# Optimization experiments

Measured on AMD Instinct MI355X. Metric: run time of the kernel, lower is better.

The kernel has to match this reference:

```python
import jax, jax.numpy as jnp
import numpy as np

T, B, V, H = 256, 256, 512, 1024


def setup_inputs() -> dict:
    key = jax.random.key(0)
    k1, k2, k3, k4 = jax.random.split(key, 4)
    # lecun_normal-like scaling for stability
    return {
        "inputs": jax.random.normal(k1, (T, B, V), dtype=jnp.float32),
        "W_xh": jax.random.normal(k2, (V, H), dtype=jnp.float32) / np.sqrt(V),
        "W_hh": jax.random.normal(k3, (H, H), dtype=jnp.float32) / np.sqrt(H),
        "b_h": jnp.zeros((H,), dtype=jnp.float32),
        "W_dense": jax.random.normal(k4, (H, V), dtype=jnp.float32) / np.sqrt(H),
        "b_dense": jnp.zeros((V,), dtype=jnp.float32),
    }


def reference(inputs, W_xh, W_hh, b_h, W_dense, b_dense):
    # Pre-compute the input projection for all timesteps (one big GEMM).
    xh = jnp.einsum("tbv,vh->tbh", inputs, W_xh) + b_h  # [T, B, H]

    def step(h, x_t):
        h_new = jnp.tanh(x_t + jnp.matmul(h, W_hh))
        return h_new, h_new

    h0 = jnp.zeros((inputs.shape[1], W_hh.shape[0]), dtype=inputs.dtype)
    state, hs = jax.lax.scan(step, h0, xh)  # hs: [T, B, H]

    outputs = jnp.einsum("tbh,hv->tbv", hs, W_dense) + b_dense  # [T, B, V]
    return outputs, state
```

## Files before the change

### kernel.cpp

```cpp
#include <hip/hip_runtime.h>


#define T_STEPS 256
#define B_SZ    256
#define V_SZ    512
#define H_SZ    1024
#define BH      (B_SZ * H_SZ)
#define M1      (T_STEPS * B_SZ)

typedef __attribute__((ext_vector_type(8))) short bf16x8;
typedef __attribute__((ext_vector_type(4))) float f32x4;

__device__ inline unsigned short bf16_rne(float f) {
    unsigned u = __float_as_uint(f);
    u += 0x7fffu + ((u >> 16) & 1u);
    return (unsigned short)(u >> 16);
}

__global__ __launch_bounds__(256, 4)
void gemm_f32_xh(const float* __restrict__ A, const float* __restrict__ Bw,
                 const float* __restrict__ bias, float* __restrict__ C)
{
    __shared__ __align__(16) float As[16][128];
    __shared__ __align__(16) float Bs[16][128];
    const int tid = threadIdx.x;
    const int tx = tid & 15, ty = tid >> 4;
    const int r0 = blockIdx.y * 128, c0 = blockIdx.x * 128;
    const int ar = tid >> 1, ak = (tid & 1) * 8;
    const int bk = tid >> 4, bc = (tid & 15) * 8;

    float acc[8][8] = {};

    for (int kc = 0; kc < V_SZ; kc += 16) {
        const float* ap = A + (size_t)(r0 + ar) * V_SZ + kc + ak;
        float4 a0 = ((const float4*)ap)[0];
        float4 a1 = ((const float4*)ap)[1];
        const float* bp = Bw + (size_t)(kc + bk) * H_SZ + c0 + bc;
        float4 b0 = ((const float4*)bp)[0];
        float4 b1 = ((const float4*)bp)[1];
        __syncthreads();
        As[ak + 0][ar] = a0.x; As[ak + 1][ar] = a0.y;
        As[ak + 2][ar] = a0.z; As[ak + 3][ar] = a0.w;
        As[ak + 4][ar] = a1.x; As[ak + 5][ar] = a1.y;
        As[ak + 6][ar] = a1.z; As[ak + 7][ar] = a1.w;
        *(float4*)&Bs[bk][bc]     = b0;
        *(float4*)&Bs[bk][bc + 4] = b1;
        __syncthreads();
#pragma unroll
        for (int kk = 0; kk < 16; ++kk) {
            float ra[8], rb[8];
            *(float4*)(ra)     = *(const float4*)&As[kk][ty * 8];
            *(float4*)(ra + 4) = *(const float4*)&As[kk][ty * 8 + 4];
            *(float4*)(rb)     = *(const float4*)&Bs[kk][tx * 8];
            *(float4*)(rb + 4) = *(const float4*)&Bs[kk][tx * 8 + 4];
#pragma unroll
            for (int i = 0; i < 8; ++i)
#pragma unroll
                for (int j = 0; j < 8; ++j)
                    acc[i][j] += ra[i] * rb[j];
        }
    }

    float4 bv0 = *(const float4*)(bias + c0 + tx * 8);
    float4 bv1 = *(const float4*)(bias + c0 + tx * 8 + 4);
#pragma unroll
    for (int i = 0; i < 8; ++i) {
        float* cp = C + (size_t)(r0 + ty * 8 + i) * H_SZ + c0 + tx * 8;
        float4 o0, o1;
        o0.x = acc[i][0] + bv0.x; o0.y = acc[i][1] + bv0.y;
        o0.z = acc[i][2] + bv0.z; o0.w = acc[i][3] + bv0.w;
        o1.x = acc[i][4] + bv1.x; o1.y = acc[i][5] + bv1.y;
        o1.z = acc[i][6] + bv1.z; o1.w = acc[i][7] + bv1.w;
        ((float4*)cp)[0] = o0;
        ((float4*)cp)[1] = o1;
    }
}

__global__ __launch_bounds__(512, 2)
void scan_gemm(const float* __restrict__ Hprev, const float* __restrict__ Whh,
               float* __restrict__ P)
{
    __shared__ __align__(16) float As[16][68];
    __shared__ __align__(16) float Bs[16][128];
    const int tid = threadIdx.x;
    const int tx = tid & 31, ty = tid >> 5;
    const int c0 = blockIdx.x * 128;
    const int r0 = blockIdx.y * 64;
    const int k0 = blockIdx.z * 128;
    const int ar = tid >> 3, ak = (tid & 7) * 2;
    const int bk = tid >> 5, bc = (tid & 31) * 4;

    float acc[4][4] = {};

    for (int kc = 0; kc < 128; kc += 16) {
        float2 a2 = *(const float2*)(Hprev + (size_t)(r0 + ar) * H_SZ + k0 + kc + ak);
        float4 b4 = *(const float4*)(Whh + (size_t)(k0 + kc + bk) * H_SZ + c0 + bc);
        __syncthreads();
        As[ak][ar]     = a2.x;
        As[ak + 1][ar] = a2.y;
        *(float4*)&Bs[bk][bc] = b4;
        __syncthreads();
#pragma unroll
        for (int kk = 0; kk < 16; ++kk) {
            float4 ra = *(const float4*)&As[kk][ty * 4];
            float4 rb = *(const float4*)&Bs[kk][tx * 4];
            acc[0][0] += ra.x * rb.x; acc[0][1] += ra.x * rb.y;
            acc[0][2] += ra.x * rb.z; acc[0][3] += ra.x * rb.w;
            acc[1][0] += ra.y * rb.x; acc[1][1] += ra.y * rb.y;
            acc[1][2] += ra.y * rb.z; acc[1][3] += ra.y * rb.w;
            acc[2][0] += ra.z * rb.x; acc[2][1] += ra.z * rb.y;
            acc[2][2] += ra.z * rb.z; acc[2][3] += ra.z * rb.w;
            acc[3][0] += ra.w * rb.x; acc[3][1] += ra.w * rb.y;
            acc[3][2] += ra.w * rb.z; acc[3][3] += ra.w * rb.w;
        }
    }

    float* pp = P + (size_t)blockIdx.z * BH;
#pragma unroll
    for (int i = 0; i < 4; ++i) {
        float4 o; o.x = acc[i][0]; o.y = acc[i][1]; o.z = acc[i][2]; o.w = acc[i][3];
        *(float4*)(pp + (size_t)(r0 + ty * 4 + i) * H_SZ + c0 + tx * 4) = o;
    }
}

__global__ __launch_bounds__(256)
void scan_reduce(const float* __restrict__ P, float* __restrict__ XH)
{
    int i = (blockIdx.x * 256 + threadIdx.x) * 4;
    float4 s = *(const float4*)(XH + i);
#pragma unroll
    for (int ks = 0; ks < 8; ++ks) {
        float4 p = *(const float4*)(P + (size_t)ks * BH + i);
        s.x += p.x; s.y += p.y; s.z += p.z; s.w += p.w;
    }
    float4 o;
    o.x = tanhf(s.x); o.y = tanhf(s.y); o.z = tanhf(s.z); o.w = tanhf(s.w);
    *(float4*)(XH + i) = o;
}

__global__ __launch_bounds__(256)
void tanh_inplace(float* __restrict__ X)
{
    int i = (blockIdx.x * 256 + threadIdx.x) * 4;
    float4 x = *(float4*)(X + i);
    float4 o;
    o.x = tanhf(x.x); o.y = tanhf(x.y); o.z = tanhf(x.z); o.w = tanhf(x.w);
    *(float4*)(X + i) = o;
}

__global__ __launch_bounds__(256)
void cvt_wdense(const float* __restrict__ Wd, unsigned short* __restrict__ WdT)
{
    __shared__ float tile[64][65];
    const int tid = threadIdx.x;
    const int kt = blockIdx.x * 64, nt = blockIdx.y * 64;
    const int kr = tid >> 2, nc = (tid & 3) * 16;
#pragma unroll
    for (int i = 0; i < 4; ++i) {
        float4 v = *(const float4*)(Wd + (size_t)(kt + kr) * V_SZ + nt + nc + i * 4);
        tile[kr][nc + i * 4 + 0] = v.x;
        tile[kr][nc + i * 4 + 1] = v.y;
        tile[kr][nc + i * 4 + 2] = v.z;
        tile[kr][nc + i * 4 + 3] = v.w;
    }
    __syncthreads();
    const int nr = tid >> 2, kc = (tid & 3) * 16;
    unsigned words[8];
#pragma unroll
    for (int j = 0; j < 8; ++j) {
        unsigned short lo = bf16_rne(tile[kc + 2 * j][nr]);
        unsigned short hi = bf16_rne(tile[kc + 2 * j + 1][nr]);
        words[j] = (unsigned)lo | ((unsigned)hi << 16);
    }
    unsigned* wp = (unsigned*)(WdT + (size_t)(nt + nr) * H_SZ + kt + kc);
    ((uint4*)wp)[0] = make_uint4(words[0], words[1], words[2], words[3]);
    ((uint4*)wp)[1] = make_uint4(words[4], words[5], words[6], words[7]);
}

__global__ __launch_bounds__(256, 2)
void gemm_out_mfma(const float* __restrict__ hs, const unsigned short* __restrict__ WdT,
                   const float* __restrict__ bias, float* __restrict__ out)
{
    __shared__ __align__(16) short As[128 * 40];
    __shared__ __align__(16) short Bs[128 * 32];
    const int tid = threadIdx.x;
    const int lane = tid & 63;
    const int w = tid >> 6;
    const int r0 = blockIdx.y * 128, c0 = blockIdx.x * 128;
    const int rw = (w >> 1) * 64, cw = (w & 1) * 64;

    const int s_row = tid & 127;
    const int s_kh  = tid >> 7;
    const int b_n   = tid >> 2;
    const int b_q   = tid & 3;

    f32x4 acc[4][4];
#pragma unroll
    for (int i = 0; i < 4; ++i)
#pragma unroll
        for (int j = 0; j < 4; ++j)
            acc[i][j] = (f32x4){0.f, 0.f, 0.f, 0.f};

    const int l15 = lane & 15, l16 = lane >> 4;

    for (int kc = 0; kc < H_SZ; kc += 32) {
        const float* ap = hs + (size_t)(r0 + s_row) * H_SZ + kc + s_kh * 16;
        float4 a0 = ((const float4*)ap)[0];
        float4 a1 = ((const float4*)ap)[1];
        float4 a2 = ((const float4*)ap)[2];
        float4 a3 = ((const float4*)ap)[3];
        unsigned pk[8];
        pk[0] = __builtin_amdgcn_perm(__float_as_uint(a0.y), __float_as_uint(a0.x), 0x07060302u);
        pk[1] = __builtin_amdgcn_perm(__float_as_uint(a0.w), __float_as_uint(a0.z), 0x07060302u);
        pk[2] = __builtin_amdgcn_perm(__float_as_uint(a1.y), __float_as_uint(a1.x), 0x07060302u);
        pk[3] = __builtin_amdgcn_perm(__float_as_uint(a1.w), __float_as_uint(a1.z), 0x07060302u);
        pk[4] = __builtin_amdgcn_perm(__float_as_uint(a2.y), __float_as_uint(a2.x), 0x07060302u);
        pk[5] = __builtin_amdgcn_perm(__float_as_uint(a2.w), __float_as_uint(a2.z), 0x07060302u);
        pk[6] = __builtin_amdgcn_perm(__float_as_uint(a3.y), __float_as_uint(a3.x), 0x07060302u);
        pk[7] = __builtin_amdgcn_perm(__float_as_uint(a3.w), __float_as_uint(a3.z), 0x07060302u);
        bf16x8 bld0 = *(const bf16x8*)(WdT + (size_t)(c0 + b_n) * H_SZ + kc + b_q * 8);
        bf16x8 bld1 = *(const bf16x8*)(WdT + (size_t)(c0 + b_n + 64) * H_SZ + kc + b_q * 8);
        __syncthreads();
        ((uint4*)&As[s_row * 40 + s_kh * 16])[0] = make_uint4(pk[0], pk[1], pk[2], pk[3]);
        ((uint4*)&As[s_row * 40 + s_kh * 16 + 8])[0] = make_uint4(pk[4], pk[5], pk[6], pk[7]);
        *(bf16x8*)(&Bs[b_n * 32 + b_q * 8]) = bld0;
        *(bf16x8*)(&Bs[(b_n + 64) * 32 + b_q * 8]) = bld1;
        __syncthreads();

        bf16x8 af[4], bf[4];
#pragma unroll
        for (int mi = 0; mi < 4; ++mi)
            af[mi] = *(const bf16x8*)(&As[(rw + mi * 16 + l15) * 40 + l16 * 8]);
#pragma unroll
        for (int ni = 0; ni < 4; ++ni)
            bf[ni] = *(const bf16x8*)(&Bs[(cw + ni * 16 + l15) * 32 + l16 * 8]);
#pragma unroll
        for (int mi = 0; mi < 4; ++mi)
#pragma unroll
            for (int ni = 0; ni < 4; ++ni)
                acc[mi][ni] = __builtin_amdgcn_mfma_f32_16x16x32_bf16(
                    af[mi], bf[ni], acc[mi][ni], 0, 0, 0);
    }

#pragma unroll
    for (int ni = 0; ni < 4; ++ni) {
        const int col = c0 + cw + ni * 16 + l15;
        const float bv = bias[col];
#pragma unroll
        for (int mi = 0; mi < 4; ++mi) {
            const int rowb = r0 + rw + mi * 16 + l16 * 4;
#pragma unroll
            for (int r = 0; r < 4; ++r)
                out[(size_t)(rowb + r) * V_SZ + col] = acc[mi][ni][r] + bv;
        }
    }
}

__global__ __launch_bounds__(256)
void copy_f4(const float* __restrict__ src, float* __restrict__ dst)
{
    int i = blockIdx.x * 256 + threadIdx.x;
    ((float4*)dst)[i] = ((const float4*)src)[i];
}

extern "C" void kernel_launch(void* const* d_in, const int* in_sizes, int n_in,
                              void* d_out, int out_size, void* d_ws, size_t ws_size,
                              hipStream_t stream)
{
    const float* inputs  = (const float*)d_in[0];
    const float* W_xh    = (const float*)d_in[1];
    const float* W_hh    = (const float*)d_in[2];
    const float* b_h     = (const float*)d_in[3];
    const float* W_dense = (const float*)d_in[4];
    const float* b_dense = (const float*)d_in[5];
    float* out = (float*)d_out;

    float* buf = (float*)d_ws;
    float* P   = out;
    unsigned short* WdT = (unsigned short*)(out + (size_t)M1 * V_SZ);

    cvt_wdense<<<dim3(H_SZ / 64, V_SZ / 64), 256, 0, stream>>>(W_dense, WdT);

    gemm_f32_xh<<<dim3(H_SZ / 128, M1 / 128), 256, 0, stream>>>(
        inputs, W_xh, b_h, buf);

    tanh_inplace<<<dim3(BH / 1024), 256, 0, stream>>>(buf);

    for (int t = 1; t < T_STEPS; ++t) {
        scan_gemm<<<dim3(8, 4, 8), 512, 0, stream>>>(
            buf + (size_t)(t - 1) * BH, W_hh, P);
        scan_reduce<<<dim3(BH / 1024), 256, 0, stream>>>(P, buf + (size_t)t * BH);
    }

    gemm_out_mfma<<<dim3(V_SZ / 128, M1 / 128), 256, 0, stream>>>(
        buf, WdT, b_dense, out);

    copy_f4<<<dim3(BH / 1024), 256, 0, stream>>>(
        buf + (size_t)(T_STEPS - 1) * BH, out + (size_t)M1 * V_SZ);
}
```

Baseline: 5.460 ms.

## Fuse recurrent scan into persistent cooperative kernel with W_hh slices in LDS

Replaces the 255 pairs of split-K scan_gemm and scan_reduce launches with one persistent cooperative kernel of 256 blocks. Each block keeps its 1024x32 column slice of W_hh resident in shared memory (128 KB) and computes a 32x32 output tile per step, fusing the add and tanh. Steps are separated by grid.sync. This removes per-step launch overhead, the partial-sum buffer traffic and the repeated reloads of W_hh, at the cost of one block per CU, 255 grid-wide barriers, and FP32 FMA math on small tiles with no MFMA.

```diff
diff --git a/kernel.cpp b/kernel.cpp
--- a/kernel.cpp
+++ b/kernel.cpp
@@ -1,4 +1,7 @@
 #include <hip/hip_runtime.h>
+#include <hip/hip_cooperative_groups.h>
+
+namespace cg = cooperative_groups;
 
 
 #define T_STEPS 256
@@ -76,76 +79,84 @@
     }
 }
 
-__global__ __launch_bounds__(512, 2)
-void scan_gemm(const float* __restrict__ Hprev, const float* __restrict__ Whh,
-               float* __restrict__ P)
-{
-    __shared__ __align__(16) float As[16][68];
-    __shared__ __align__(16) float Bs[16][128];
+__global__ __launch_bounds__(256, 1)
+void scan_coop(const float* __restrict__ Whh, float* buf)
+{
+    __shared__ __align__(16) float Ws[H_SZ][32];
+    __shared__ __align__(16) float hs[4][2][8][36];
+
     const int tid = threadIdx.x;
-    const int tx = tid & 31, ty = tid >> 5;
-    const int c0 = blockIdx.x * 128;
-    const int r0 = blockIdx.y * 64;
-    const int k0 = blockIdx.z * 128;
-    const int ar = tid >> 3, ak = (tid & 7) * 2;
-    const int bk = tid >> 5, bc = (tid & 31) * 4;
-
-    float acc[4][4] = {};
-
-    for (int kc = 0; kc < 128; kc += 16) {
-        float2 a2 = *(const float2*)(Hprev + (size_t)(r0 + ar) * H_SZ + k0 + kc + ak);
-        float4 b4 = *(const float4*)(Whh + (size_t)(k0 + kc + bk) * H_SZ + c0 + bc);
-        __syncthreads();
-        As[ak][ar]     = a2.x;
-        As[ak + 1][ar] = a2.y;
-        *(float4*)&Bs[bk][bc] = b4;
-        __syncthreads();
-#pragma unroll
-        for (int kk = 0; kk < 16; ++kk) {
-            float4 ra = *(const float4*)&As[kk][ty * 4];
-            float4 rb = *(const float4*)&Bs[kk][tx * 4];
-            acc[0][0] += ra.x * rb.x; acc[0][1] += ra.x * rb.y;
-            acc[0][2] += ra.x * rb.z; acc[0][3] += ra.x * rb.w;
-            acc[1][0] += ra.y * rb.x; acc[1][1] += ra.y * rb.y;
-            acc[1][2] += ra.y * rb.z; acc[1][3] += ra.y * rb.w;
-            acc[2][0] += ra.z * rb.x; acc[2][1] += ra.z * rb.y;
-            acc[2][2] += ra.z * rb.z; acc[2][3] += ra.z * rb.w;
-            acc[3][0] += ra.w * rb.x; acc[3][1] += ra.w * rb.y;
-            acc[3][2] += ra.w * rb.z; acc[3][3] += ra.w * rb.w;
+    const int bid = blockIdx.x;
+    const int r0 = (bid >> 5) * 32;
+    const int c0 = (bid & 31) * 32;
+    const int w = tid >> 6;
+    const int lane = tid & 63;
+    const int rl = lane >> 3;
+    const int c4 = lane & 7;
+    const int wr0 = r0 + w * 8;
+
+    cg::grid_group grid = cg::this_grid();
+
+    for (int it = 0; it < 32; ++it) {
+        int idx = it * 256 + tid;
+        int k = idx >> 3, cq = idx & 7;
+        *(float4*)&Ws[k][cq * 4] =
+            *(const float4*)(Whh + (size_t)k * H_SZ + c0 + cq * 4);
+    }
+    {
+        int r = tid >> 3, cq = tid & 7;
+        float* p = buf + (size_t)(r0 + r) * H_SZ + c0 + cq * 4;
+        float4 x = *(float4*)p;
+        float4 o;
+        o.x = tanhf(x.x); o.y = tanhf(x.y); o.z = tanhf(x.z); o.w = tanhf(x.w);
+        *(float4*)p = o;
+    }
+    __syncthreads();
+    grid.sync();
+
+    for (int t = 1; t < T_STEPS; ++t) {
+        const float* hprev = buf + (size_t)(t - 1) * BH;
+        float* hcur = buf + (size_t)t * BH;
+
+        const float* arow = hprev + (size_t)(wr0 + rl) * H_SZ;
+        float4 xh = *(const float4*)(hcur + (size_t)(wr0 + rl) * H_SZ + c0 + c4 * 4);
+
+        float4 acc; acc.x = acc.y = acc.z = acc.w = 0.f;
+
+        float4 pre = *(const float4*)(arow + c4 * 4);
+        *(float4*)&hs[w][0][rl][c4 * 4] = pre;
+
+        for (int ch = 0; ch < 32; ++ch) {
+            const int cur = ch & 1;
+            float4 nxt;
+            if (ch < 31)
+                nxt = *(const float4*)(arow + (ch + 1) * 32 + c4 * 4);
+#pragma unroll
+            for (int kq = 0; kq < 8; ++kq) {
+                float4 a = *(const float4*)&hs[w][cur][rl][kq * 4];
+                const int kb = ch * 32 + kq * 4;
+                float4 b0 = *(const float4*)&Ws[kb + 0][c4 * 4];
+                float4 b1 = *(const float4*)&Ws[kb + 1][c4 * 4];
+                float4 b2 = *(const float4*)&Ws[kb + 2][c4 * 4];
+                float4 b3 = *(const float4*)&Ws[kb + 3][c4 * 4];
+                acc.x += a.x * b0.x + a.y * b1.x + a.z * b2.x + a.w * b3.x;
+                acc.y += a.x * b0.y + a.y * b1.y + a.z * b2.y + a.w * b3.y;
+                acc.z += a.x * b0.z + a.y * b1.z + a.z * b2.z + a.w * b3.z;
+                acc.w += a.x * b0.w + a.y * b1.w + a.z * b2.w + a.w * b3.w;
+            }
+            if (ch < 31)
+                *(float4*)&hs[w][cur ^ 1][rl][c4 * 4] = nxt;
         }
-    }
-
-    float* pp = P + (size_t)blockIdx.z * BH;
-#pragma unroll
-    for (int i = 0; i < 4; ++i) {
-        float4 o; o.x = acc[i][0]; o.y = acc[i][1]; o.z = acc[i][2]; o.w = acc[i][3];
-        *(float4*)(pp + (size_t)(r0 + ty * 4 + i) * H_SZ + c0 + tx * 4) = o;
-    }
-}
-
-__global__ __launch_bounds__(256)
-void scan_reduce(const float* __restrict__ P, float* __restrict__ XH)
-{
-    int i = (blockIdx.x * 256 + threadIdx.x) * 4;
-    float4 s = *(const float4*)(XH + i);
-#pragma unroll
-    for (int ks = 0; ks < 8; ++ks) {
-        float4 p = *(const float4*)(P + (size_t)ks * BH + i);
-        s.x += p.x; s.y += p.y; s.z += p.z; s.w += p.w;
-    }
-    float4 o;
-    o.x = tanhf(s.x); o.y = tanhf(s.y); o.z = tanhf(s.z); o.w = tanhf(s.w);
-    *(float4*)(XH + i) = o;
-}
-
-__global__ __launch_bounds__(256)
-void tanh_inplace(float* __restrict__ X)
-{
-    int i = (blockIdx.x * 256 + threadIdx.x) * 4;
-    float4 x = *(float4*)(X + i);
-    float4 o;
-    o.x = tanhf(x.x); o.y = tanhf(x.y); o.z = tanhf(x.z); o.w = tanhf(x.w);
-    *(float4*)(X + i) = o;
+
+        float4 o;
+        o.x = tanhf(xh.x + acc.x);
+        o.y = tanhf(xh.y + acc.y);
+        o.z = tanhf(xh.z + acc.z);
+        o.w = tanhf(xh.w + acc.w);
+        *(float4*)(hcur + (size_t)(wr0 + rl) * H_SZ + c0 + c4 * 4) = o;
+
+        grid.sync();
+    }
 }
 
 __global__ __launch_bounds__(256)
@@ -227,19 +238,19 @@
         *(bf16x8*)(&Bs[(b_n + 64) * 32 + b_q * 8]) = bld1;
         __syncthreads();
 
-        bf16x8 af[4], bf[4];
+        bf16x8 af[4], bfr[4];
 #pragma unroll
         for (int mi = 0; mi < 4; ++mi)
             af[mi] = *(const bf16x8*)(&As[(rw + mi * 16 + l15) * 40 + l16 * 8]);
 #pragma unroll
         for (int ni = 0; ni < 4; ++ni)
-            bf[ni] = *(const bf16x8*)(&Bs[(cw + ni * 16 + l15) * 32 + l16 * 8]);
+            bfr[ni] = *(const bf16x8*)(&Bs[(cw + ni * 16 + l15) * 32 + l16 * 8]);
 #pragma unroll
         for (int mi = 0; mi < 4; ++mi)
 #pragma unroll
             for (int ni = 0; ni < 4; ++ni)
                 acc[mi][ni] = __builtin_amdgcn_mfma_f32_16x16x32_bf16(
-                    af[mi], bf[ni], acc[mi][ni], 0, 0, 0);
+                    af[mi], bfr[ni], acc[mi][ni], 0, 0, 0);
     }
 
 #pragma unroll
@@ -276,7 +287,6 @@
     float* out = (float*)d_out;
 
     float* buf = (float*)d_ws;
-    float* P   = out;
     unsigned short* WdT = (unsigned short*)(out + (size_t)M1 * V_SZ);
 
     cvt_wdense<<<dim3(H_SZ / 64, V_SZ / 64), 256, 0, stream>>>(W_dense, WdT);
@@ -284,12 +294,10 @@
     gemm_f32_xh<<<dim3(H_SZ / 128, M1 / 128), 256, 0, stream>>>(
         inputs, W_xh, b_h, buf);
 
-    tanh_inplace<<<dim3(BH / 1024), 256, 0, stream>>>(buf);
-
-    for (int t = 1; t < T_STEPS; ++t) {
-        scan_gemm<<<dim3(8, 4, 8), 512, 0, stream>>>(
-            buf + (size_t)(t - 1) * BH, W_hh, P);
-        scan_reduce<<<dim3(BH / 1024), 256, 0, stream>>>(P, buf + (size_t)t * BH);
+    {
+        void* args[] = {(void*)&W_hh, (void*)&buf};
+        hipLaunchCooperativeKernel((const void*)scan_coop, dim3(256), dim3(256),
+                                   args, 0, stream);
     }
 
     gemm_out_mfma<<<dim3(V_SZ / 128, M1 / 128), 256, 0, stream>>>(
```

New measurement: 11.97 ms. 2.19x slower.
